# Performance work log

Measured on AMD Instinct MI355X. Metric: run time of the kernel, lower is better.

The kernel has to match this reference:

```python
import jax, jax.numpy as jnp
import numpy as np

D_MODEL = 1024
NUM_HEADS = 16
HEAD_DIM = D_MODEL // NUM_HEADS


def setup_inputs() -> dict:
    key = jax.random.key(0)
    ks = jax.random.split(key, 9)
    s = 1.0 / np.sqrt(D_MODEL)
    x = jax.random.normal(ks[0], (2, 2048, D_MODEL), dtype=jnp.float32)
    Wq = jax.random.normal(ks[1], (D_MODEL, D_MODEL), dtype=jnp.float32) * s
    Wk = jax.random.normal(ks[2], (D_MODEL, D_MODEL), dtype=jnp.float32) * s
    Wv = jax.random.normal(ks[3], (D_MODEL, D_MODEL), dtype=jnp.float32) * s
    Wo = jax.random.normal(ks[4], (D_MODEL, D_MODEL), dtype=jnp.float32) * s
    bq = jax.random.normal(ks[5], (D_MODEL,), dtype=jnp.float32) * s
    bk = jax.random.normal(ks[6], (D_MODEL,), dtype=jnp.float32) * s
    bv = jax.random.normal(ks[7], (D_MODEL,), dtype=jnp.float32) * s
    bo = jax.random.normal(ks[8], (D_MODEL,), dtype=jnp.float32) * s
    return {"x": x, "Wq": Wq, "bq": bq, "Wk": Wk, "bk": bk, "Wv": Wv, "bv": bv, "Wo": Wo, "bo": bo}


def reference(x, Wq, bq, Wk, bk, Wv, bv, Wo, bo):
    B, S, D = x.shape
    H, Hd = NUM_HEADS, HEAD_DIM
    # QKV projections
    q = (x @ Wq + bq).reshape(B, S, H, Hd).transpose(0, 2, 1, 3)  # [B,H,S,Hd]
    k = (x @ Wk + bk).reshape(B, S, H, Hd).transpose(0, 2, 1, 3)
    v = (x @ Wv + bv).reshape(B, S, H, Hd).transpose(0, 2, 1, 3)
    scores = jnp.einsum("bhqd,bhkd->bhqk", q, k) / jnp.sqrt(jnp.float32(Hd))
    attn = jax.nn.softmax(scores, axis=-1)
    out = jnp.einsum("bhqk,bhkd->bhqd", attn, v)  # [B,H,S,Hd]
    out = out.transpose(0, 2, 1, 3).reshape(B, S, D)
    return out @ Wo + bo
```

## Files before the change

### kernel.cpp

```cpp
#include <hip/hip_runtime.h>
#include <hip/hip_bf16.h>


typedef unsigned short u16;

#define D_MODEL 1024
#define NHEAD 16
#define HDIM 64
#define BATCH 2
#define SEQ 2048
#define MTOT (BATCH * SEQ)

#define QSCALE 0.18033688011112042f

using frag_ab = __attribute__((ext_vector_type(8))) short;
using frag_s4 = __attribute__((ext_vector_type(4))) short;
using frag_cd = __attribute__((ext_vector_type(4))) float;
using f32x2   = __attribute__((ext_vector_type(2))) float;
using u16x8   = __attribute__((ext_vector_type(8))) unsigned short;

__device__ __forceinline__ u16 f2u(float f) {
    union { float f; unsigned int i; } x;
    x.f = f;
    unsigned int r = x.i + 0x7fffu + ((x.i >> 16) & 1u);
    return (u16)(r >> 16);
}
__device__ __forceinline__ unsigned int pkrn(float a, float b) {
    union { __hip_bfloat162 h; unsigned int u; } c;
    c.h = __float22bfloat162_rn(float2{a, b});
    return c.u;
}
__device__ __forceinline__ float fexp2(float x) {
#if __has_builtin(__builtin_amdgcn_exp2f)
    return __builtin_amdgcn_exp2f(x);
#else
    float r;
    asm("v_exp_f32 %0, %1" : "=v"(r) : "v"(x));
    return r;
#endif
}

__global__ void prep(const float* __restrict__ W0, const float* __restrict__ W1,
                     const float* __restrict__ W2, const float* __restrict__ W3,
                     const float* __restrict__ X, u16* __restrict__ Wt,
                     u16* __restrict__ Xb) {
    const int z = blockIdx.z;
    const int tx = threadIdx.x, ty = threadIdx.y;
    const int tid = ty * 32 + tx;
    if (z < 4) {
        __shared__ u16 t[32][33];
        const float* W = (z == 0) ? W0 : (z == 1) ? W1 : (z == 2) ? W2 : W3;
        u16* o = Wt + (size_t)z * D_MODEL * D_MODEL;
        int n0 = blockIdx.x * 32, k0 = blockIdx.y * 32;
        #pragma unroll
        for (int i = ty; i < 32; i += 8) t[i][tx] = f2u(W[(size_t)(k0 + i) * D_MODEL + n0 + tx]);
        __syncthreads();
        const int r = tid >> 3, c = tid & 7;
        ushort4 o4;
        o4.x = t[4 * c + 0][r]; o4.y = t[4 * c + 1][r];
        o4.z = t[4 * c + 2][r]; o4.w = t[4 * c + 3][r];
        *(ushort4*)&o[(size_t)(n0 + r) * D_MODEL + k0 + 4 * c] = o4;
    } else {
        size_t base = ((size_t)(blockIdx.y * 32 + blockIdx.x) * 256 + tid) * 16;
        #pragma unroll
        for (int c = 0; c < 4; ++c) {
            float4 v = *(const float4*)&X[base + c * 4];
            ushort4 o;
            o.x = f2u(v.x); o.y = f2u(v.y); o.z = f2u(v.z); o.w = f2u(v.w);
            *(ushort4*)&Xb[base + c * 4] = o;
        }
    }
}

__launch_bounds__(256, 4)
__global__ void gemm_qkvt(const u16* __restrict__ xb, const u16* __restrict__ Wt,
                          const float* __restrict__ bq, const float* __restrict__ bk,
                          const float* __restrict__ bv, u16* __restrict__ QKw,
                          u16* __restrict__ Vtw) {
    constexpr int BK = 64;
    __shared__ __attribute__((aligned(16))) u16 SM[128 * 136];
    u16* As = SM;
    u16* Bs = SM + 128 * BK;

    const int tid = threadIdx.x;
    const int w = tid >> 6;
    const int lane = tid & 63;
    const int lrow = lane & 15, lquad = lane >> 4;
    const size_t WSZ = (size_t)D_MODEL * D_MODEL;
    const size_t TSZ = (size_t)MTOT * D_MODEL;

    const int bid0 = blockIdx.x;
    const int bid = (bid0 & 7) * 96 + (bid0 >> 3);
    const bool vt = bid >= 512;
    const int z = vt ? 2 : (bid >> 8);
    const int t = vt ? (bid - 512) : (bid & 255);
    const int n0 = vt ? (t & 31) * 128 : (t & 7) * 128;
    const int m0 = vt ? (t >> 5) * 128 : (t >> 3) * 128;
    const u16* Ap = vt ? (Wt + 2 * WSZ) : xb;
    const u16* Bp = vt ? xb : (Wt + (size_t)z * WSZ);
    const float* bias = vt ? bv : (z ? bk : bq);

    frag_cd acc[4][4];
    #pragma unroll
    for (int i = 0; i < 4; i++)
        #pragma unroll
        for (int j = 0; j < 4; j++) acc[i][j] = (frag_cd){0.f, 0.f, 0.f, 0.f};

    const int wm = (w >> 1) * 64, wn = (w & 1) * 64;

    for (int k0 = 0; k0 < D_MODEL; k0 += BK) {
        __syncthreads();
        #pragma unroll
        for (int it = 0; it < 4; ++it) {
            int c = it * 256 + tid;
            int r = c >> 3, c8 = c & 7;
            const u16* ga = Ap + (size_t)(m0 + r) * D_MODEL + k0 + c8 * 8;
            char* la = (char*)As + (it * 256 + w * 64) * 16;
            __builtin_amdgcn_global_load_lds((const __attribute__((address_space(1))) void*)ga,
                                             (__attribute__((address_space(3))) void*)la, 16, 0, 0);
            const u16* gb = Bp + (size_t)(n0 + r) * D_MODEL + k0 + c8 * 8;
            char* lb = (char*)Bs + (it * 256 + w * 64) * 16;
            __builtin_amdgcn_global_load_lds((const __attribute__((address_space(1))) void*)gb,
                                             (__attribute__((address_space(3))) void*)lb, 16, 0, 0);
        }
        __syncthreads();

        #pragma unroll
        for (int kc = 0; kc < 2; ++kc) {
            frag_ab av[4], bvv[4];
            #pragma unroll
            for (int i = 0; i < 4; i++)
                av[i] = *(const frag_ab*)&As[(wm + i * 16 + lrow) * BK + kc * 32 + lquad * 8];
            #pragma unroll
            for (int j = 0; j < 4; j++)
                bvv[j] = *(const frag_ab*)&Bs[(wn + j * 16 + lrow) * BK + kc * 32 + lquad * 8];
            #pragma unroll
            for (int i = 0; i < 4; i++)
                #pragma unroll
                for (int j = 0; j < 4; j++)
                    acc[i][j] = __builtin_amdgcn_mfma_f32_16x16x32_bf16(av[i], bvv[j], acc[i][j], 0, 0, 0);
        }
    }

    const float scale = (!vt && z == 0) ? QSCALE : 1.0f;
    __syncthreads();
    #pragma unroll
    for (int j = 0; j < 4; j++) {
        int col = wn + j * 16 + lrow;
        float bn = vt ? 0.f : bias[n0 + col];
        #pragma unroll
        for (int i = 0; i < 4; i++) {
            #pragma unroll
            for (int rr = 0; rr < 4; ++rr) {
                int row = wm + i * 16 + lquad * 4 + rr;
                float v = vt ? (acc[i][j][rr] + bias[m0 + row])
                             : (acc[i][j][rr] + bn) * scale;
                SM[row * 136 + col] = f2u(v);
            }
        }
    }
    __syncthreads();
    #pragma unroll
    for (int it = 0; it < 8; ++it) {
        int idx = it * 256 + tid;
        int row = idx >> 4, seg = idx & 15;
        u16x8 v8 = *(const u16x8*)&SM[row * 136 + seg * 8];
        if (!vt) {
            int gm = m0 + row;
            int gc = n0 + seg * 8;
            int b = gm >> 11, s = gm & (SEQ - 1);
            int h = gc >> 6, d0 = gc & (HDIM - 1);
            u16* oz = QKw + (size_t)z * TSZ;
            *(u16x8*)&oz[(((size_t)(b * NHEAD + h)) * SEQ + s) * HDIM + d0] = v8;
        } else {
            int gm = m0 + row;
            int h = gm >> 6, d = gm & (HDIM - 1);
            int gc = n0 + seg * 8;
            int b = gc >> 11, s0 = gc & (SEQ - 1);
            *(u16x8*)&Vtw[(((size_t)(b * NHEAD + h)) * HDIM + d) * SEQ + s0] = v8;
        }
    }
}

__launch_bounds__(256, 4)
__global__ void gemm_out(const u16* __restrict__ A, const u16* __restrict__ Wt,
                         const float* __restrict__ bias, float* __restrict__ out) {
    constexpr int BK = 64;
    __shared__ __attribute__((aligned(16))) u16 SM[64 * 68 * 2];
    u16* As = SM;
    u16* Bs = SM + 64 * BK;

    const int tid = threadIdx.x;
    const int w = tid >> 6;
    const int lane = tid & 63;
    const int lrow = lane & 15, lquad = lane >> 4;
    const int L0 = blockIdx.y * 16 + blockIdx.x;
    const int L = (L0 & 7) * 128 + (L0 >> 3);
    const int m0 = (L >> 4) * 64, n0 = (L & 15) * 64;

    frag_cd acc[2][2];
    #pragma unroll
    for (int i = 0; i < 2; i++)
        #pragma unroll
        for (int j = 0; j < 2; j++) acc[i][j] = (frag_cd){0.f, 0.f, 0.f, 0.f};

    const int wm = (w >> 1) * 32, wn = (w & 1) * 32;

    for (int k0 = 0; k0 < D_MODEL; k0 += BK) {
        __syncthreads();
        #pragma unroll
        for (int it = 0; it < 2; ++it) {
            int c = it * 256 + tid;
            int r = c >> 3, c8 = c & 7;
            const u16* ga = A + (size_t)(m0 + r) * D_MODEL + k0 + c8 * 8;
            char* la = (char*)As + (it * 256 + w * 64) * 16;
            __builtin_amdgcn_global_load_lds((const __attribute__((address_space(1))) void*)ga,
                                             (__attribute__((address_space(3))) void*)la, 16, 0, 0);
            const u16* gb = Wt + (size_t)(n0 + r) * D_MODEL + k0 + c8 * 8;
            char* lb = (char*)Bs + (it * 256 + w * 64) * 16;
            __builtin_amdgcn_global_load_lds((const __attribute__((address_space(1))) void*)gb,
                                             (__attribute__((address_space(3))) void*)lb, 16, 0, 0);
        }
        __syncthreads();

        #pragma unroll
        for (int kc = 0; kc < 2; ++kc) {
            frag_ab av[2], bvv[2];
            #pragma unroll
            for (int i = 0; i < 2; i++)
                av[i] = *(const frag_ab*)&As[(wm + i * 16 + lrow) * BK + kc * 32 + lquad * 8];
            #pragma unroll
            for (int j = 0; j < 2; j++)
                bvv[j] = *(const frag_ab*)&Bs[(wn + j * 16 + lrow) * BK + kc * 32 + lquad * 8];
            #pragma unroll
            for (int i = 0; i < 2; i++)
                #pragma unroll
                for (int j = 0; j < 2; j++)
                    acc[i][j] = __builtin_amdgcn_mfma_f32_16x16x32_bf16(av[i], bvv[j], acc[i][j], 0, 0, 0);
        }
    }

    float* Tf = (float*)SM;
    __syncthreads();
    #pragma unroll
    for (int j = 0; j < 2; j++) {
        int col = wn + j * 16 + lrow;
        float bvf = bias[n0 + col];
        #pragma unroll
        for (int i = 0; i < 2; i++)
            #pragma unroll
            for (int rr = 0; rr < 4; ++rr) {
                int row = wm + i * 16 + lquad * 4 + rr;
                Tf[row * 68 + col] = acc[i][j][rr] + bvf;
            }
    }
    __syncthreads();
    #pragma unroll
    for (int it = 0; it < 4; ++it) {
        int idx = it * 256 + tid;
        int row = idx >> 4, seg = idx & 15;
        float4 v = *(const float4*)&Tf[row * 68 + seg * 4];
        *(float4*)&out[(size_t)(m0 + row) * D_MODEL + n0 + seg * 4] = v;
    }
}

__launch_bounds__(512, 4)
__global__ void attn_kernel(const u16* __restrict__ Q, const u16* __restrict__ K,
                            const u16* __restrict__ Vt, u16* __restrict__ O) {
    __shared__ __attribute__((aligned(16))) u16 SMEM[32768];
    u16* Ks = SMEM;
    u16* Vs = SMEM + 16384;

    const int tid = threadIdx.x;
    const int w = tid >> 6;
    const int lane = tid & 63;
    const int lrow = lane & 15, lquad = lane >> 4;
    const int qg = w & 3;
    const int kh = w >> 2;

    const int L = blockIdx.y * 16 + blockIdx.x;
    const int xcd = L & 7, off = L >> 3;
    const int bh = xcd * 4 + (off >> 4);
    const int q0 = (off & 15) * 128;

    const size_t base = (size_t)bh * SEQ * HDIM;
    const u16* Qg = Q + base;
    const u16* Kg = K + base;
    const u16* Vg = Vt + base;

    frag_ab qf[2][2];
    #pragma unroll
    for (int g = 0; g < 2; ++g)
        #pragma unroll
        for (int kc = 0; kc < 2; ++kc)
            qf[g][kc] = *(const frag_ab*)&Qg[(size_t)(q0 + (qg + g * 4) * 16 + lrow) * HDIM + kc * 32 + lquad * 8];

    frag_cd accOT[2][4];
    #pragma unroll
    for (int g = 0; g < 2; ++g)
        #pragma unroll
        for (int df = 0; df < 4; df++) accOT[g][df] = (frag_cd){0.f, 0.f, 0.f, 0.f};
    f32x2 la0 = (f32x2){0.f, 0.f}, la1 = (f32x2){0.f, 0.f};

    const u16* gk[4]; const u16* gv[4]; char* lk[4]; char* lv[4];
    #pragma unroll
    for (int i = 0; i < 4; ++i) {
        const int c = i * 512 + tid;
        gk[i] = Kg + ((c >> 3) * HDIM + (((c & 7) ^ ((c >> 3) & 7)) << 3));
        gv[i] = Vg + ((size_t)(c >> 5) * SEQ + (((c & 31) ^ ((c >> 5) & 7)) << 3));
        lk[i] = (char*)Ks + (i * 512 + w * 64) * 16;
        lv[i] = (char*)Vs + (i * 512 + w * 64) * 16;
    }

    const u16* kb0 = Ks + (kh * 128 + lrow) * 64 + (((0 + lquad) ^ (lrow & 7)) << 3);
    const u16* kb1 = Ks + (kh * 128 + lrow) * 64 + (((4 + lquad) ^ (lrow & 7)) << 3);
    const u16* vb[8];
    #pragma unroll
    for (int cm = 0; cm < 8; ++cm) {
        const int gc = ((kh * 8 + cm) << 1) + (lquad >> 1);
        vb[cm] = Vs + lrow * 256 + ((gc ^ (lrow & 7)) << 3) + (lquad & 1) * 4;
    }

    for (int kt = 0; kt < SEQ / 256; ++kt) {
        __syncthreads();
        #pragma unroll
        for (int i = 0; i < 4; ++i) {
            __builtin_amdgcn_global_load_lds((const __attribute__((address_space(1))) void*)gk[i],
                                             (__attribute__((address_space(3))) void*)lk[i], 16, 0, 0);
            __builtin_amdgcn_global_load_lds((const __attribute__((address_space(1))) void*)gv[i],
                                             (__attribute__((address_space(3))) void*)lv[i], 16, 0, 0);
            gk[i] += 256 * HDIM;
            gv[i] += 256;
        }
        __syncthreads();

        #pragma unroll
        for (int cm = 0; cm < 8; ++cm) {
            frag_cd sc0 = (frag_cd){0.f, 0.f, 0.f, 0.f};
            frag_cd sc1 = (frag_cd){0.f, 0.f, 0.f, 0.f};
            __builtin_amdgcn_s_setprio(1);
            {
                frag_ab kf0 = *(const frag_ab*)(kb0 + cm * 1024);
                frag_ab kf1 = *(const frag_ab*)(kb1 + cm * 1024);
                sc0 = __builtin_amdgcn_mfma_f32_16x16x32_bf16(kf0, qf[0][0], sc0, 0, 0, 0);
                sc1 = __builtin_amdgcn_mfma_f32_16x16x32_bf16(kf0, qf[1][0], sc1, 0, 0, 0);
                sc0 = __builtin_amdgcn_mfma_f32_16x16x32_bf16(kf1, qf[0][1], sc0, 0, 0, 0);
                sc1 = __builtin_amdgcn_mfma_f32_16x16x32_bf16(kf1, qf[1][1], sc1, 0, 0, 0);
            }
            __builtin_amdgcn_s_setprio(0);

            frag_s4 pk0, pk1;
            {
                float e0 = fexp2(sc0[0]), e1 = fexp2(sc0[1]);
                float e2 = fexp2(sc0[2]), e3 = fexp2(sc0[3]);
                f32x2 a = {e0, e1}, b2 = {e2, e3};
                la0 += a + b2;
                union { frag_s4 s; unsigned int u[2]; } pu;
                pu.u[0] = pkrn(e0, e1);
                pu.u[1] = pkrn(e2, e3);
                pk0 = pu.s;
            }
            {
                float e0 = fexp2(sc1[0]), e1 = fexp2(sc1[1]);
                float e2 = fexp2(sc1[2]), e3 = fexp2(sc1[3]);
                f32x2 a = {e0, e1}, b2 = {e2, e3};
                la1 += a + b2;
                union { frag_s4 s; unsigned int u[2]; } pu;
                pu.u[0] = pkrn(e0, e1);
                pu.u[1] = pkrn(e2, e3);
                pk1 = pu.s;
            }

            __builtin_amdgcn_s_setprio(1);
            {
                const u16* vp = vb[cm];
                #pragma unroll
                for (int df = 0; df < 4; df++) {
                    frag_s4 vf = *(const frag_s4*)(vp + df * 16 * 256);
                    accOT[0][df] = __builtin_amdgcn_mfma_f32_16x16x16bf16_1k(vf, pk0, accOT[0][df], 0, 0, 0);
                    accOT[1][df] = __builtin_amdgcn_mfma_f32_16x16x16bf16_1k(vf, pk1, accOT[1][df], 0, 0, 0);
                }
            }
            __builtin_amdgcn_s_setprio(0);
        }
    }

    float s0 = la0[0] + la0[1];
    s0 += __shfl_xor(s0, 16);
    s0 += __shfl_xor(s0, 32);
    float s1 = la1[0] + la1[1];
    s1 += __shfl_xor(s1, 16);
    s1 += __shfl_xor(s1, 32);

    float* comb = (float*)SMEM;
    float* lsum = (float*)SMEM + 128 * 68;
    __syncthreads();
    if (kh) {
        #pragma unroll
        for (int g = 0; g < 2; ++g) {
            float* crow = comb + ((qg + g * 4) * 16 + lrow) * 68;
            #pragma unroll
            for (int df = 0; df < 4; df++)
                *(float4*)&crow[df * 16 + lquad * 4] =
                    (float4){accOT[g][df][0], accOT[g][df][1], accOT[g][df][2], accOT[g][df][3]};
        }
        if (lquad == 0) {
            lsum[qg * 16 + lrow] = s0;
            lsum[(qg + 4) * 16 + lrow] = s1;
        }
    }
    __syncthreads();
    if (!kh) {
        const int b = bh >> 4, h = bh & (NHEAD - 1);
        #pragma unroll
        for (int g = 0; g < 2; ++g) {
            const float* crow = comb + ((qg + g * 4) * 16 + lrow) * 68;
            #pragma unroll
            for (int df = 0; df < 4; df++) {
                float4 c = *(const float4*)&crow[df * 16 + lquad * 4];
                accOT[g][df][0] += c.x; accOT[g][df][1] += c.y;
                accOT[g][df][2] += c.z; accOT[g][df][3] += c.w;
            }
            float lacc = (g ? s1 : s0) + lsum[(qg + g * 4) * 16 + lrow];

            const int s = q0 + (qg + g * 4) * 16 + lrow;
            const float inv = 1.0f / lacc;
            u16* orow = O + ((size_t)(b * SEQ + s)) * D_MODEL + h * HDIM;
            #pragma unroll
            for (int df = 0; df < 4; df++) {
                union { unsigned int u[2]; ushort4 s4; } o;
                o.u[0] = pkrn(accOT[g][df][0] * inv, accOT[g][df][1] * inv);
                o.u[1] = pkrn(accOT[g][df][2] * inv, accOT[g][df][3] * inv);
                *(ushort4*)&orow[df * 16 + lquad * 4] = o.s4;
            }
        }
    }
}

extern "C" void kernel_launch(void* const* d_in, const int* in_sizes, int n_in,
                              void* d_out, int out_size, void* d_ws, size_t ws_size,
                              hipStream_t stream) {
    const float* x  = (const float*)d_in[0];
    const float* Wq = (const float*)d_in[1];
    const float* bq = (const float*)d_in[2];
    const float* Wk = (const float*)d_in[3];
    const float* bk = (const float*)d_in[4];
    const float* Wv = (const float*)d_in[5];
    const float* bv = (const float*)d_in[6];
    const float* Wo = (const float*)d_in[7];
    const float* bo = (const float*)d_in[8];

    u16* ws = (u16*)d_ws;
    const size_t WSZ = (size_t)D_MODEL * D_MODEL;
    const size_t TSZ = (size_t)MTOT * D_MODEL;
    u16* xb  = ws;
    u16* Wt  = ws + 4 * WSZ;
    u16* QKw = ws + 8 * WSZ;
    u16* Vtw = QKw + 2 * TSZ;
    u16* Aw  = Vtw + TSZ;

    prep<<<dim3(32, 32, 5), dim3(32, 8), 0, stream>>>(Wq, Wk, Wv, Wo, x, Wt, xb);
    gemm_qkvt<<<dim3(768), 256, 0, stream>>>(xb, Wt, bq, bk, bv, QKw, Vtw);
    attn_kernel<<<dim3(16, 32), 512, 0, stream>>>(QKw, QKw + TSZ, Vtw, Aw);
    gemm_out<<<dim3(16, 64), 256, 0, stream>>>(Aw, Wt + 3 * WSZ, bo, (float*)d_out);
}
```

Measured before the change: 199.8 us.

## Use 16x16x32 MFMA for PV by pairing key chunks into K=32 fragments

```diff
diff --git a/kernel.cpp b/kernel.cpp
--- a/kernel.cpp
+++ b/kernel.cpp
@@ -312,13 +312,17 @@
         lv[i] = (char*)Vs + (i * 512 + w * 64) * 16;
     }
 
-    const u16* kb0 = Ks + (kh * 128 + lrow) * 64 + (((0 + lquad) ^ (lrow & 7)) << 3);
-    const u16* kb1 = Ks + (kh * 128 + lrow) * 64 + (((4 + lquad) ^ (lrow & 7)) << 3);
-    const u16* vb[8];
-    #pragma unroll
-    for (int cm = 0; cm < 8; ++cm) {
-        const int gc = ((kh * 8 + cm) << 1) + (lquad >> 1);
-        vb[cm] = Vs + lrow * 256 + ((gc ^ (lrow & 7)) << 3) + (lquad & 1) * 4;
+    const int rA = kh * 128 + 8 * (lrow >> 2) + (lrow & 3);
+    const int rB = rA + 4;
+    const u16* kA0 = Ks + rA * 64 + (((0 + lquad) ^ (lrow & 3)) << 3);
+    const u16* kA1 = Ks + rA * 64 + (((4 + lquad) ^ (lrow & 3)) << 3);
+    const u16* kB0 = Ks + rB * 64 + (((0 + lquad) ^ ((lrow & 3) + 4)) << 3);
+    const u16* kB1 = Ks + rB * 64 + (((4 + lquad) ^ ((lrow & 3) + 4)) << 3);
+    const u16* vb[4];
+    #pragma unroll
+    for (int pr = 0; pr < 4; ++pr) {
+        const int gc = kh * 16 + pr * 4 + lquad;
+        vb[pr] = Vs + lrow * 256 + ((gc ^ (lrow & 7)) << 3);
     }
 
     for (int kt = 0; kt < SEQ / 256; ++kt) {
@@ -335,50 +339,62 @@
         __syncthreads();
 
         #pragma unroll
-        for (int cm = 0; cm < 8; ++cm) {
-            frag_cd sc0 = (frag_cd){0.f, 0.f, 0.f, 0.f};
-            frag_cd sc1 = (frag_cd){0.f, 0.f, 0.f, 0.f};
+        for (int pr = 0; pr < 4; ++pr) {
+            frag_cd sA0 = (frag_cd){0.f, 0.f, 0.f, 0.f};
+            frag_cd sA1 = (frag_cd){0.f, 0.f, 0.f, 0.f};
+            frag_cd sB0 = (frag_cd){0.f, 0.f, 0.f, 0.f};
+            frag_cd sB1 = (frag_cd){0.f, 0.f, 0.f, 0.f};
             __builtin_amdgcn_s_setprio(1);
             {
-                frag_ab kf0 = *(const frag_ab*)(kb0 + cm * 1024);
-                frag_ab kf1 = *(const frag_ab*)(kb1 + cm * 1024);
-                sc0 = __builtin_amdgcn_mfma_f32_16x16x32_bf16(kf0, qf[0][0], sc0, 0, 0, 0);
-                sc1 = __builtin_amdgcn_mfma_f32_16x16x32_bf16(kf0, qf[1][0], sc1, 0, 0, 0);
-                sc0 = __builtin_amdgcn_mfma_f32_16x16x32_bf16(kf1, qf[0][1], sc0, 0, 0, 0);
-                sc1 = __builtin_amdgcn_mfma_f32_16x16x32_bf16(kf1, qf[1][1], sc1, 0, 0, 0);
+                frag_ab f0 = *(const frag_ab*)(kA0 + pr * 2048);
+                frag_ab f1 = *(const frag_ab*)(kA1 + pr * 2048);
+                sA0 = __builtin_amdgcn_mfma_f32_16x16x32_bf16(f0, qf[0][0], sA0, 0, 0, 0);
+                sA1 = __builtin_amdgcn_mfma_f32_16x16x32_bf16(f0, qf[1][0], sA1, 0, 0, 0);
+                sA0 = __builtin_amdgcn_mfma_f32_16x16x32_bf16(f1, qf[0][1], sA0, 0, 0, 0);
+                sA1 = __builtin_amdgcn_mfma_f32_16x16x32_bf16(f1, qf[1][1], sA1, 0, 0, 0);
+                frag_ab g0 = *(const frag_ab*)(kB0 + pr * 2048);
+                frag_ab g1 = *(const frag_ab*)(kB1 + pr * 2048);
+                sB0 = __builtin_amdgcn_mfma_f32_16x16x32_bf16(g0, qf[0][0], sB0, 0, 0, 0);
+                sB1 = __builtin_amdgcn_mfma_f32_16x16x32_bf16(g0, qf[1][0], sB1, 0, 0, 0);
+                sB0 = __builtin_amdgcn_mfma_f32_16x16x32_bf16(g1, qf[0][1], sB0, 0, 0, 0);
+                sB1 = __builtin_amdgcn_mfma_f32_16x16x32_bf16(g1, qf[1][1], sB1, 0, 0, 0);
             }
             __builtin_amdgcn_s_setprio(0);
 
-            frag_s4 pk0, pk1;
+            frag_ab pb0, pb1;
             {
-                float e0 = fexp2(sc0[0]), e1 = fexp2(sc0[1]);
-                float e2 = fexp2(sc0[2]), e3 = fexp2(sc0[3]);
-                f32x2 a = {e0, e1}, b2 = {e2, e3};
-                la0 += a + b2;
-                union { frag_s4 s; unsigned int u[2]; } pu;
-                pu.u[0] = pkrn(e0, e1);
-                pu.u[1] = pkrn(e2, e3);
-                pk0 = pu.s;
+                float e0 = fexp2(sA0[0]), e1 = fexp2(sA0[1]);
+                float e2 = fexp2(sA0[2]), e3 = fexp2(sA0[3]);
+                float e4 = fexp2(sB0[0]), e5 = fexp2(sB0[1]);
+                float e6 = fexp2(sB0[2]), e7 = fexp2(sB0[3]);
+                f32x2 a = {e0, e1}, b2 = {e2, e3}, c2 = {e4, e5}, d2 = {e6, e7};
+                la0 += (a + b2) + (c2 + d2);
+                union { frag_ab s; unsigned int u[4]; } pu;
+                pu.u[0] = pkrn(e0, e1); pu.u[1] = pkrn(e2, e3);
+                pu.u[2] = pkrn(e4, e5); pu.u[3] = pkrn(e6, e7);
+                pb0 = pu.s;
             }
             {
-                float e0 = fexp2(sc1[0]), e1 = fexp2(sc1[1]);
-                float e2 = fexp2(sc1[2]), e3 = fexp2(sc1[3]);
-                f32x2 a = {e0, e1}, b2 = {e2, e3};
-                la1 += a + b2;
-                union { frag_s4 s; unsigned int u[2]; } pu;
-                pu.u[0] = pkrn(e0, e1);
-                pu.u[1] = pkrn(e2, e3);
-                pk1 = pu.s;
+                float e0 = fexp2(sA1[0]), e1 = fexp2(sA1[1]);
+                float e2 = fexp2(sA1[2]), e3 = fexp2(sA1[3]);
+                float e4 = fexp2(sB1[0]), e5 = fexp2(sB1[1]);
+                float e6 = fexp2(sB1[2]), e7 = fexp2(sB1[3]);
+                f32x2 a = {e0, e1}, b2 = {e2, e3}, c2 = {e4, e5}, d2 = {e6, e7};
+                la1 += (a + b2) + (c2 + d2);
+                union { frag_ab s; unsigned int u[4]; } pu;
+                pu.u[0] = pkrn(e0, e1); pu.u[1] = pkrn(e2, e3);
+                pu.u[2] = pkrn(e4, e5); pu.u[3] = pkrn(e6, e7);
+                pb1 = pu.s;
             }
 
             __builtin_amdgcn_s_setprio(1);
             {
-                const u16* vp = vb[cm];
+                const u16* vp = vb[pr];
                 #pragma unroll
                 for (int df = 0; df < 4; df++) {
-                    frag_s4 vf = *(const frag_s4*)(vp + df * 16 * 256);
-                    accOT[0][df] = __builtin_amdgcn_mfma_f32_16x16x16bf16_1k(vf, pk0, accOT[0][df], 0, 0, 0);
-                    accOT[1][df] = __builtin_amdgcn_mfma_f32_16x16x16bf16_1k(vf, pk1, accOT[1][df], 0, 0, 0);
+                    frag_ab vf = *(const frag_ab*)(vp + df * 16 * 256);
+                    accOT[0][df] = __builtin_amdgcn_mfma_f32_16x16x32_bf16(vf, pb0, accOT[0][df], 0, 0, 0);
+                    accOT[1][df] = __builtin_amdgcn_mfma_f32_16x16x32_bf16(vf, pb1, accOT[1][df], 0, 0, 0);
                 }
             }
             __builtin_amdgcn_s_setprio(0);
```

Result: no change. 196.9 us (-1.5%).
